# Kernel tuning notes

Hardware: AMD Instinct MI355X
Metric: run time of the kernel (lower is better)

The kernel has to match this reference:

```python
import jax, jax.numpy as jnp
import numpy as np

# 4D convolution via lax.conv_general_dilated with 4 spatial dims.
# Layout: input (N, C, D, H, W, T), kernel (O, I, d, h, w, t).
DN = ('NCDHWT', 'OIDHWT', 'NCDHWT')


def conv4d(x, w, b, pad):
    # torch Conv2d/Conv4d is cross-correlation, matching lax.conv_general_dilated
    y = jax.lax.conv_general_dilated(
        x, w, window_strides=(1, 1, 1, 1),
        padding=[(pad, pad)] * 4, dimension_numbers=DN)
    return y + b.reshape(1, -1, 1, 1, 1, 1)


def _kaiming(key, shape):
    fan_out = shape[0] * int(np.prod(shape[2:]))
    std = np.sqrt(2.0 / fan_out)
    return (jax.random.normal(key, shape, dtype=jnp.float32) * std).astype(jnp.float32)


def setup_inputs() -> dict:
    key = jax.random.key(0)
    ks = jax.random.split(key, 11)
    B, W, H = 256, 16, 16
    corr = jax.random.normal(ks[0], (B, W * H, W, H), dtype=jnp.float32)
    w1 = _kaiming(ks[1], (1, 1, 17, 17, 9, 9))
    w2 = _kaiming(ks[2], (1, 1, 7, 7, 7, 7))
    w3 = _kaiming(ks[3], (1, 1, 5, 5, 5, 5))
    w4 = _kaiming(ks[4], (1, 1, 3, 3, 3, 3))
    w5 = _kaiming(ks[5], (1, 1, 8, 8, 1, 1))
    b1 = jax.random.normal(ks[6], (1,), dtype=jnp.float32) * 0.01
    b2 = jax.random.normal(ks[7], (1,), dtype=jnp.float32) * 0.01
    b3 = jax.random.normal(ks[8], (1,), dtype=jnp.float32) * 0.01
    b4 = jax.random.normal(ks[9], (1,), dtype=jnp.float32) * 0.01
    b5 = jax.random.normal(ks[10], (1,), dtype=jnp.float32) * 0.01
    return {"corr": corr, "w1": w1, "b1": b1, "w2": w2, "b2": b2,
            "w3": w3, "b3": b3, "w4": w4, "b4": b4, "w5": w5, "b5": b5}


def reference(corr, w1, b1, w2, b2, w3, b3, w4, b4, w5, b5):
    B, HW, W, H = corr.shape
    x = corr.reshape(B, 1, W, H, W, H)          # (B,1,16,16,16,16)
    x = jax.nn.relu(conv4d(x, w1, b1, 4))       # (B,1, 8, 8,16,16)
    x = jax.nn.relu(conv4d(x, w2, b2, 3))
    x = jax.nn.relu(conv4d(x, w3, b3, 2))
    x = jax.nn.relu(conv4d(x, w4, b4, 1))
    out = jax.nn.sigmoid(conv4d(x, w5, b5, 0))  # (B,1, 1, 1,16,16)
    return out.reshape(B, 1, W, H)
```

## Files before the change

### kernel.cpp

```cpp
#include <hip/hip_runtime.h>
#include <math.h>


typedef short bf16x8 __attribute__((ext_vector_type(8)));
typedef float f32x4 __attribute__((ext_vector_type(4)));
typedef unsigned int u32x4 __attribute__((ext_vector_type(4)));

#define XTS 64
#define NROWS 396
#define ZROW 384
#define TTS 72

__device__ __forceinline__ int xts(int row, int col) {
  return row * XTS + (col ^ ((row & 7) << 3));
}

__device__ __forceinline__ unsigned short f2bf(float f) {
  unsigned int u = __float_as_uint(f);
  u += 0x7fffu + ((u >> 16) & 1u);
  return (unsigned short)(u >> 16);
}

template <int KSZ, int PAD>
__device__ __forceinline__ void build_mid(const float* __restrict__ w,
                                          unsigned short* __restrict__ Bg, int gid) {
  const int lane = gid & 63;
  const int n_tile = (gid >> 6) & 3;
  const int chunk = (gid >> 8) & 1;
  const int tap = gid >> 9;
  const int kw = tap / KSZ, kt = tap - kw * KSZ;
  const int dh_o = n_tile * 16 + (lane & 15);
  const int d_o = dh_o >> 3, h_o = dh_o & 7;
  const int kbase = chunk * 32 + (lane >> 4) * 8;
  unsigned int pk[4];
#pragma unroll
  for (int p = 0; p < 4; ++p) {
    unsigned short half[2];
#pragma unroll
    for (int s = 0; s < 2; ++s) {
      const int k = kbase + p * 2 + s;
      const int d_i = k >> 3, h_i = k & 7;
      const int kd = d_i - d_o + PAD, kh = h_i - h_o + PAD;
      float v = 0.f;
      if (kd >= 0 && kd < KSZ && kh >= 0 && kh < KSZ)
        v = w[((kd * KSZ + kh) * KSZ + kw) * KSZ + kt];
      half[s] = f2bf(v);
    }
    pk[p] = (unsigned int)half[0] | ((unsigned int)half[1] << 16);
  }
  *(int4*)(Bg + (size_t)gid * 8) = make_int4(pk[0], pk[1], pk[2], pk[3]);
}

__global__ __launch_bounds__(256) void build_all(const float* __restrict__ w1,
                                                 const float* __restrict__ w2,
                                                 const float* __restrict__ w3,
                                                 const float* __restrict__ w4,
                                                 unsigned short* __restrict__ Bg1,
                                                 unsigned short* __restrict__ Bg2,
                                                 unsigned short* __restrict__ Bg3,
                                                 unsigned short* __restrict__ Bg4) {
  const int bid = blockIdx.x, tid = threadIdx.x;
  if (bid < 648) {
    const int gid = bid * 256 + tid;
    const int lane = gid & 63;
    const int n_tile = (gid >> 6) & 3;
    const int chunk = (gid >> 8) & 7;
    const int kwkt = gid >> 11;
    const int kw = kwkt / 9, kt = kwkt - kw * 9;
    const int dh_o = n_tile * 16 + (lane & 15);
    const int d_o = dh_o >> 3, h_o = dh_o & 7;
    const int kbase = chunk * 32 + (lane >> 4) * 8;
    unsigned int pk[4];
#pragma unroll
    for (int p = 0; p < 4; ++p) {
      unsigned short half[2];
#pragma unroll
      for (int s = 0; s < 2; ++s) {
        const int k = kbase + p * 2 + s;
        const int d_i = k >> 4, h_i = k & 15;
        const int kd = d_i - d_o + 4, kh = h_i - h_o + 4;
        float v = 0.f;
        if (kd >= 0 && kd < 17 && kh >= 0 && kh < 17)
          v = w1[((kd * 17 + kh) * 9 + kw) * 9 + kt];
        half[s] = f2bf(v);
      }
      pk[p] = (unsigned int)half[0] | ((unsigned int)half[1] << 16);
    }
    *(int4*)(Bg1 + (size_t)gid * 8) = make_int4(pk[0], pk[1], pk[2], pk[3]);
  } else if (bid < 746) {
    build_mid<7, 3>(w2, Bg2, (bid - 648) * 256 + tid);
  } else if (bid < 796) {
    build_mid<5, 2>(w3, Bg3, (bid - 746) * 256 + tid);
  } else {
    build_mid<3, 1>(w4, Bg4, (bid - 796) * 256 + tid);
  }
}

__device__ __forceinline__ void l1_loadA(const unsigned short* XT, const int (&arb)[4],
                                         int kt, int tl, int quad, int chalf,
                                         bf16x8 (&A)[4]) {
  const int sw = ((tl + kt) & 7) << 3;
  const int c = (quad * 8 + chalf * 32) ^ sw;
  const int ko = kt * XTS;
#pragma unroll
  for (int m = 0; m < 4; ++m)
    A[m] = *(const bf16x8*)&XT[arb[m] + ko + c];
}

__device__ __forceinline__ void l1_loadB(const unsigned short* __restrict__ Bt, int kt,
                                         bf16x8 (&B)[8]) {
#pragma unroll
  for (int c = 0; c < 2; ++c)
#pragma unroll
    for (int n = 0; n < 4; ++n)
      B[c * 4 + n] = *(const bf16x8*)(Bt + (size_t)kt * 16384 + c * 2048 + n * 512);
}

__device__ __forceinline__ void mfma_half(const bf16x8 (&A)[4], const bf16x8* B,
                                          f32x4 (&acc)[4][4]) {
  __builtin_amdgcn_s_setprio(1);
#pragma unroll
  for (int m = 0; m < 4; ++m)
#pragma unroll
    for (int n = 0; n < 4; ++n)
      acc[m][n] = __builtin_amdgcn_mfma_f32_16x16x32_bf16(A[m], B[n], acc[m][n], 0, 0, 0);
  __builtin_amdgcn_s_setprio(0);
}

__global__ __launch_bounds__(256) void conv_l1_mfma(const float* __restrict__ x,
                                                    const unsigned short* __restrict__ Bg,
                                                    float* __restrict__ P) {
  __shared__ __align__(16) unsigned short XT[NROWS * XTS];
  const int bx = blockIdx.x;
  const int b = bx >> 1, khalf = bx & 1;
  const int tid = threadIdx.x;
  const int lane = tid & 63, wave = tid >> 6;
  const int quad = lane >> 4, tl = lane & 15;
  const float* xb = x + (size_t)b * 65536;
  f32x4 acc[4][4] = {};

  for (int j = tid; j < (NROWS * XTS) / 8; j += 256)
    *(int4*)&XT[j * 8] = make_int4(0, 0, 0, 0);
  __syncthreads();

  for (int qq = 0; qq < 2; ++qq) {
    const int q = khalf * 2 + qq;
    if (qq) __syncthreads();
#pragma unroll
    for (int it = 0; it < 8; ++it) {
      const int i = tid + it * 256;
      const int dhp = i >> 6, wtq = i & 63;
      const int r0 = (wtq >> 2) * 24 + (wtq & 3) * 4 + 4;
      const float4 ra = *(const float4*)(xb + (size_t)(q * 64 + 2 * dhp) * 256 + wtq * 4);
      const float4 rb =
          *(const float4*)(xb + (size_t)(q * 64 + 2 * dhp + 1) * 256 + wtq * 4);
      const float a0[4] = {ra.x, ra.y, ra.z, ra.w};
      const float a1[4] = {rb.x, rb.y, rb.z, rb.w};
#pragma unroll
      for (int j = 0; j < 4; ++j) {
        const unsigned int p = (unsigned int)f2bf(a0[j]) | ((unsigned int)f2bf(a1[j]) << 16);
        *(unsigned int*)&XT[xts(r0 + j, dhp * 2)] = p;
      }
    }
    __syncthreads();

    const unsigned short* Bt = Bg + (size_t)(q * 2) * 2048 + lane * 8;
    for (int kw = 0; kw < 9; ++kw) {
      int arb[4];
#pragma unroll
      for (int m = 0; m < 4; ++m) {
        const int w_i = wave * 4 + m + kw - 4;
        arb[m] = (((unsigned)w_i < 16u) ? (w_i * 24 + tl) : ZROW) * XTS;
      }
      bf16x8 B0[8], B1[8];
      l1_loadB(Bt, 0, B0);
#pragma unroll
      for (int kt = 0; kt < 9; ++kt) {
        bf16x8* Bc = (kt & 1) ? B1 : B0;
        bf16x8* Bn = (kt & 1) ? B0 : B1;
        if (kt < 8) l1_loadB(Bt, kt + 1, *(bf16x8(*)[8])Bn);
        bf16x8 A[4];
        l1_loadA(XT, arb, kt, tl, quad, 0, A);
        mfma_half(A, Bc, acc);
        l1_loadA(XT, arb, kt, tl, quad, 1, A);
        mfma_half(A, Bc + 4, acc);
      }
      Bt += 9 * 16384;
    }
  }

  float* Pb = P + (size_t)(khalf * 256 + b) * 16384;
#pragma unroll
  for (int m = 0; m < 4; ++m)
#pragma unroll
    for (int n = 0; n < 4; ++n) {
      const int dh_o = n * 16 + tl;
      const int wt0 = wave * 64 + m * 16 + quad * 4;
      *(float4*)&Pb[(size_t)dh_o * 256 + wt0] = *(const float4*)&acc[m][n];
    }
}

template <int KSZ, int PAD>
__device__ __forceinline__ void run_layer(unsigned short* XT,
                                          const unsigned short* __restrict__ Bg,
                                          const float bias, int mw, int nh, int lane,
                                          int quad, int tl) {
  f32x4 acc[4][2] = {};
  const unsigned short* BgL = Bg + lane * 8;
#pragma unroll
  for (int kt = 0; kt < KSZ; ++kt) {
    const int t_i = tl + kt - PAD;
    const bool tv = (unsigned)t_i < 16u;
    bf16x8 Aw[2][4];
#pragma unroll
    for (int m = 0; m < 4; ++m) {
      const int w_i = mw * 4 + m - PAD;
      const int row = (tv && (unsigned)w_i < 16u) ? (w_i * 16 + t_i) : 256;
      const int ro = row * TTS + quad * 8;
      Aw[0][m] = *(const bf16x8*)&XT[ro];
      Aw[1][m] = *(const bf16x8*)&XT[ro + 32];
    }
    bf16x8 Bb[2][4];
#pragma unroll
    for (int c = 0; c < 2; ++c)
#pragma unroll
      for (int n = 0; n < 2; ++n)
        Bb[0][c * 2 + n] =
            *(const bf16x8*)(BgL + (((size_t)(kt * 2 + c) * 4 + (nh * 2 + n)) << 9));
#pragma unroll
    for (int kw = 0; kw < KSZ; ++kw) {
      const int cur = kw & 1, nxt = cur ^ 1;
      if (kw + 1 < KSZ) {
        const int kwkt = (kw + 1) * KSZ + kt;
#pragma unroll
        for (int c = 0; c < 2; ++c)
#pragma unroll
          for (int n = 0; n < 2; ++n)
            Bb[nxt][c * 2 + n] =
                *(const bf16x8*)(BgL + (((size_t)(kwkt * 2 + c) * 4 + (nh * 2 + n)) << 9));
      }
      __builtin_amdgcn_s_setprio(1);
#pragma unroll
      for (int c = 0; c < 2; ++c)
#pragma unroll
        for (int m = 0; m < 4; ++m)
#pragma unroll
          for (int n = 0; n < 2; ++n)
            acc[m][n] = __builtin_amdgcn_mfma_f32_16x16x32_bf16(
                Aw[c][(kw + m) & 3], Bb[cur][c * 2 + n], acc[m][n], 0, 0, 0);
      __builtin_amdgcn_s_setprio(0);
      if (kw + 1 < KSZ) {
        const int w_i = mw * 4 + 4 + kw - PAD;
        const int row = (tv && (unsigned)w_i < 16u) ? (w_i * 16 + t_i) : 256;
        const int ro = row * TTS + quad * 8;
        Aw[0][kw & 3] = *(const bf16x8*)&XT[ro];
        Aw[1][kw & 3] = *(const bf16x8*)&XT[ro + 32];
      }
    }
  }
  __syncthreads();
#pragma unroll
  for (int m = 0; m < 4; ++m)
#pragma unroll
    for (int n = 0; n < 2; ++n) {
      const int col = (nh * 2 + n) * 16 + tl;
      const int wt0 = mw * 64 + m * 16 + quad * 4;
#pragma unroll
      for (int j = 0; j < 4; ++j)
        XT[(wt0 + j) * TTS + col] = f2bf(fmaxf(acc[m][n][j] + bias, 0.f));
    }
  __syncthreads();
}

__global__ __launch_bounds__(512) void tail_fused(const float* __restrict__ P,
                                                  const unsigned short* __restrict__ Bg2,
                                                  const unsigned short* __restrict__ Bg3,
                                                  const unsigned short* __restrict__ Bg4,
                                                  const float* __restrict__ b1,
                                                  const float* __restrict__ b2,
                                                  const float* __restrict__ b3,
                                                  const float* __restrict__ b4,
                                                  const float* __restrict__ w5,
                                                  const float* __restrict__ b5,
                                                  float* __restrict__ out) {
  __shared__ __align__(16) unsigned short XT[257 * TTS];
  const int b = blockIdx.x;
  const int tid = threadIdx.x;
  const int lane = tid & 63, wave = tid >> 6;
  const int quad = lane >> 4, tl = lane & 15;
  const int mw = wave >> 1, nh = wave & 1;
  const float* p0 = P + (size_t)b * 16384;
  const float* p1 = p0 + (size_t)256 * 16384;
  const float bias1 = b1[0];

  if (tid < 9) *(int4*)&XT[256 * TTS + tid * 8] = make_int4(0, 0, 0, 0);
#pragma unroll
  for (int it = 0; it < 4; ++it) {
    const int i = tid + it * 512;
    const int dhp = i >> 6, wtq = i & 63;
    const size_t off0 = (size_t)(2 * dhp) * 256 + wtq * 4;
    const float4 r0a = *(const float4*)(p0 + off0);
    const float4 r0b = *(const float4*)(p1 + off0);
    const float4 r1a = *(const float4*)(p0 + off0 + 256);
    const float4 r1b = *(const float4*)(p1 + off0 + 256);
    float a0[4] = {r0a.x + r0b.x, r0a.y + r0b.y, r0a.z + r0b.z, r0a.w + r0b.w};
    float a1[4] = {r1a.x + r1b.x, r1a.y + r1b.y, r1a.z + r1b.z, r1a.w + r1b.w};
#pragma unroll
    for (int j = 0; j < 4; ++j) {
      const unsigned short lo = f2bf(fmaxf(a0[j] + bias1, 0.f));
      const unsigned short hi = f2bf(fmaxf(a1[j] + bias1, 0.f));
      const unsigned int p = (unsigned int)lo | ((unsigned int)hi << 16);
      *(unsigned int*)&XT[(wtq * 4 + j) * TTS + dhp * 2] = p;
    }
  }
  __syncthreads();

  run_layer<7, 3>(XT, Bg2, b2[0], mw, nh, lane, quad, tl);
  run_layer<5, 2>(XT, Bg3, b3[0], mw, nh, lane, quad, tl);
  run_layer<3, 1>(XT, Bg4, b4[0], mw, nh, lane, quad, tl);

  if (tid < 256) {
    const int wt = tid;
    float s = b5[0];
    const unsigned short* row = &XT[wt * TTS];
#pragma unroll
    for (int k8 = 0; k8 < 8; ++k8) {
      const u32x4 v = *(const u32x4*)&row[k8 * 8];
      const unsigned int uu[4] = {(unsigned int)v.x, (unsigned int)v.y, (unsigned int)v.z,
                                  (unsigned int)v.w};
#pragma unroll
      for (int p = 0; p < 4; ++p) {
        const float lo = __uint_as_float(uu[p] << 16);
        const float hi = __uint_as_float(uu[p] & 0xFFFF0000u);
        s += lo * w5[k8 * 8 + p * 2] + hi * w5[k8 * 8 + p * 2 + 1];
      }
    }
    out[(size_t)b * 256 + wt] = 1.f / (1.f + expf(-s));
  }
}

extern "C" void kernel_launch(void* const* d_in, const int* in_sizes, int n_in,
                              void* d_out, int out_size, void* d_ws, size_t ws_size,
                              hipStream_t stream) {
  const float* corr = (const float*)d_in[0];
  const float* w1 = (const float*)d_in[1];
  const float* b1 = (const float*)d_in[2];
  const float* w2 = (const float*)d_in[3];
  const float* b2 = (const float*)d_in[4];
  const float* w3 = (const float*)d_in[5];
  const float* b3 = (const float*)d_in[6];
  const float* w4 = (const float*)d_in[7];
  const float* b4 = (const float*)d_in[8];
  const float* w5 = (const float*)d_in[9];
  const float* b5 = (const float*)d_in[10];

  float* P = (float*)d_ws;
  unsigned short* Bg1 = (unsigned short*)((char*)d_ws + (64u << 20));
  unsigned short* Bg2 = Bg1 + (size_t)81 * 8 * 4 * 64 * 8;
  unsigned short* Bg3 = Bg2 + (size_t)49 * 2 * 4 * 64 * 8;
  unsigned short* Bg4 = Bg3 + (size_t)25 * 2 * 4 * 64 * 8;

  build_all<<<814, 256, 0, stream>>>(w1, w2, w3, w4, Bg1, Bg2, Bg3, Bg4);
  conv_l1_mfma<<<512, 256, 0, stream>>>(corr, Bg1, P);
  tail_fused<<<256, 512, 0, stream>>>(P, Bg2, Bg3, Bg4, b1, b2, b3, b4, w5, b5,
                                      (float*)d_out);
}
```

Before: 257.7 us.

## Fuse layer-1 conv into tail kernel, dropping the split-K partial buffer

Merges the layer-1 MFMA conv into the fused tail kernel, one 512-thread block per batch element. The 8 waves split the output columns (nh) instead of splitting K across two blocks, and the layer-1 result goes straight to LDS as bf16. This removes the fp32 partial-sum write and read-back through global memory and one kernel launch. In exchange the grid drops from 512 to 256 blocks, each block runs all four K quarters serially, and the larger LDS footprint may reduce occupancy.

```diff
diff --git a/kernel.cpp b/kernel.cpp
--- a/kernel.cpp
+++ b/kernel.cpp
@@ -107,97 +107,24 @@
     A[m] = *(const bf16x8*)&XT[arb[m] + ko + c];
 }
 
-__device__ __forceinline__ void l1_loadB(const unsigned short* __restrict__ Bt, int kt,
-                                         bf16x8 (&B)[8]) {
+__device__ __forceinline__ void l1_loadB2(const unsigned short* __restrict__ Bt, int kt,
+                                          bf16x8 (&B)[4]) {
 #pragma unroll
   for (int c = 0; c < 2; ++c)
 #pragma unroll
-    for (int n = 0; n < 4; ++n)
-      B[c * 4 + n] = *(const bf16x8*)(Bt + (size_t)kt * 16384 + c * 2048 + n * 512);
-}
-
-__device__ __forceinline__ void mfma_half(const bf16x8 (&A)[4], const bf16x8* B,
-                                          f32x4 (&acc)[4][4]) {
+    for (int n = 0; n < 2; ++n)
+      B[c * 2 + n] = *(const bf16x8*)(Bt + (size_t)kt * 16384 + c * 2048 + n * 512);
+}
+
+__device__ __forceinline__ void mfma_half2(const bf16x8 (&A)[4], const bf16x8* B,
+                                           f32x4 (&acc)[4][2]) {
   __builtin_amdgcn_s_setprio(1);
 #pragma unroll
   for (int m = 0; m < 4; ++m)
 #pragma unroll
-    for (int n = 0; n < 4; ++n)
+    for (int n = 0; n < 2; ++n)
       acc[m][n] = __builtin_amdgcn_mfma_f32_16x16x32_bf16(A[m], B[n], acc[m][n], 0, 0, 0);
   __builtin_amdgcn_s_setprio(0);
-}
-
-__global__ __launch_bounds__(256) void conv_l1_mfma(const float* __restrict__ x,
-                                                    const unsigned short* __restrict__ Bg,
-                                                    float* __restrict__ P) {
-  __shared__ __align__(16) unsigned short XT[NROWS * XTS];
-  const int bx = blockIdx.x;
-  const int b = bx >> 1, khalf = bx & 1;
-  const int tid = threadIdx.x;
-  const int lane = tid & 63, wave = tid >> 6;
-  const int quad = lane >> 4, tl = lane & 15;
-  const float* xb = x + (size_t)b * 65536;
-  f32x4 acc[4][4] = {};
-
-  for (int j = tid; j < (NROWS * XTS) / 8; j += 256)
-    *(int4*)&XT[j * 8] = make_int4(0, 0, 0, 0);
-  __syncthreads();
-
-  for (int qq = 0; qq < 2; ++qq) {
-    const int q = khalf * 2 + qq;
-    if (qq) __syncthreads();
-#pragma unroll
-    for (int it = 0; it < 8; ++it) {
-      const int i = tid + it * 256;
-      const int dhp = i >> 6, wtq = i & 63;
-      const int r0 = (wtq >> 2) * 24 + (wtq & 3) * 4 + 4;
-      const float4 ra = *(const float4*)(xb + (size_t)(q * 64 + 2 * dhp) * 256 + wtq * 4);
-      const float4 rb =
-          *(const float4*)(xb + (size_t)(q * 64 + 2 * dhp + 1) * 256 + wtq * 4);
-      const float a0[4] = {ra.x, ra.y, ra.z, ra.w};
-      const float a1[4] = {rb.x, rb.y, rb.z, rb.w};
-#pragma unroll
-      for (int j = 0; j < 4; ++j) {
-        const unsigned int p = (unsigned int)f2bf(a0[j]) | ((unsigned int)f2bf(a1[j]) << 16);
-        *(unsigned int*)&XT[xts(r0 + j, dhp * 2)] = p;
-      }
-    }
-    __syncthreads();
-
-    const unsigned short* Bt = Bg + (size_t)(q * 2) * 2048 + lane * 8;
-    for (int kw = 0; kw < 9; ++kw) {
-      int arb[4];
-#pragma unroll
-      for (int m = 0; m < 4; ++m) {
-        const int w_i = wave * 4 + m + kw - 4;
-        arb[m] = (((unsigned)w_i < 16u) ? (w_i * 24 + tl) : ZROW) * XTS;
-      }
-      bf16x8 B0[8], B1[8];
-      l1_loadB(Bt, 0, B0);
-#pragma unroll
-      for (int kt = 0; kt < 9; ++kt) {
-        bf16x8* Bc = (kt & 1) ? B1 : B0;
-        bf16x8* Bn = (kt & 1) ? B0 : B1;
-        if (kt < 8) l1_loadB(Bt, kt + 1, *(bf16x8(*)[8])Bn);
-        bf16x8 A[4];
-        l1_loadA(XT, arb, kt, tl, quad, 0, A);
-        mfma_half(A, Bc, acc);
-        l1_loadA(XT, arb, kt, tl, quad, 1, A);
-        mfma_half(A, Bc + 4, acc);
-      }
-      Bt += 9 * 16384;
-    }
-  }
-
-  float* Pb = P + (size_t)(khalf * 256 + b) * 16384;
-#pragma unroll
-  for (int m = 0; m < 4; ++m)
-#pragma unroll
-    for (int n = 0; n < 4; ++n) {
-      const int dh_o = n * 16 + tl;
-      const int wt0 = wave * 64 + m * 16 + quad * 4;
-      *(float4*)&Pb[(size_t)dh_o * 256 + wt0] = *(const float4*)&acc[m][n];
-    }
 }
 
 template <int KSZ, int PAD>
@@ -272,52 +199,94 @@
   __syncthreads();
 }
 
-__global__ __launch_bounds__(512) void tail_fused(const float* __restrict__ P,
-                                                  const unsigned short* __restrict__ Bg2,
-                                                  const unsigned short* __restrict__ Bg3,
-                                                  const unsigned short* __restrict__ Bg4,
-                                                  const float* __restrict__ b1,
-                                                  const float* __restrict__ b2,
-                                                  const float* __restrict__ b3,
-                                                  const float* __restrict__ b4,
-                                                  const float* __restrict__ w5,
-                                                  const float* __restrict__ b5,
-                                                  float* __restrict__ out) {
-  __shared__ __align__(16) unsigned short XT[257 * TTS];
+__global__ __launch_bounds__(512) void net_fused(const float* __restrict__ x,
+                                                 const unsigned short* __restrict__ Bg1,
+                                                 const unsigned short* __restrict__ Bg2,
+                                                 const unsigned short* __restrict__ Bg3,
+                                                 const unsigned short* __restrict__ Bg4,
+                                                 const float* __restrict__ b1,
+                                                 const float* __restrict__ b2,
+                                                 const float* __restrict__ b3,
+                                                 const float* __restrict__ b4,
+                                                 const float* __restrict__ w5,
+                                                 const float* __restrict__ b5,
+                                                 float* __restrict__ out) {
+  __shared__ __align__(16) unsigned short XT[NROWS * XTS];
   const int b = blockIdx.x;
   const int tid = threadIdx.x;
   const int lane = tid & 63, wave = tid >> 6;
   const int quad = lane >> 4, tl = lane & 15;
-  const int mw = wave >> 1, nh = wave & 1;
-  const float* p0 = P + (size_t)b * 16384;
-  const float* p1 = p0 + (size_t)256 * 16384;
+  const int g = wave >> 1, nh = wave & 1;
+  const float* xb = x + (size_t)b * 65536;
   const float bias1 = b1[0];
-
+  f32x4 acc[4][2] = {};
+
+  for (int j = tid; j < (NROWS * XTS) / 8; j += 512)
+    *(int4*)&XT[j * 8] = make_int4(0, 0, 0, 0);
+  __syncthreads();
+
+  for (int q = 0; q < 4; ++q) {
+    if (q) __syncthreads();
+#pragma unroll
+    for (int it = 0; it < 4; ++it) {
+      const int i = tid + it * 512;
+      const int dhp = i >> 6, wtq = i & 63;
+      const int r0 = (wtq >> 2) * 24 + (wtq & 3) * 4 + 4;
+      const float4 ra = *(const float4*)(xb + (size_t)(q * 64 + 2 * dhp) * 256 + wtq * 4);
+      const float4 rb =
+          *(const float4*)(xb + (size_t)(q * 64 + 2 * dhp + 1) * 256 + wtq * 4);
+      const float a0[4] = {ra.x, ra.y, ra.z, ra.w};
+      const float a1[4] = {rb.x, rb.y, rb.z, rb.w};
+#pragma unroll
+      for (int j = 0; j < 4; ++j) {
+        const unsigned int p = (unsigned int)f2bf(a0[j]) | ((unsigned int)f2bf(a1[j]) << 16);
+        *(unsigned int*)&XT[xts(r0 + j, dhp * 2)] = p;
+      }
+    }
+    __syncthreads();
+
+    const unsigned short* Bt = Bg1 + (size_t)(q * 2) * 2048 + (nh * 2) * 512 + lane * 8;
+    for (int kw = 0; kw < 9; ++kw) {
+      int arb[4];
+#pragma unroll
+      for (int m = 0; m < 4; ++m) {
+        const int w_i = g * 4 + m + kw - 4;
+        arb[m] = (((unsigned)w_i < 16u) ? (w_i * 24 + tl) : ZROW) * XTS;
+      }
+      bf16x8 B0[4], B1[4];
+      l1_loadB2(Bt, 0, B0);
+#pragma unroll
+      for (int kt = 0; kt < 9; ++kt) {
+        bf16x8* Bc = (kt & 1) ? B1 : B0;
+        bf16x8* Bn = (kt & 1) ? B0 : B1;
+        if (kt < 8) l1_loadB2(Bt, kt + 1, *(bf16x8(*)[4])Bn);
+        bf16x8 A[4];
+        l1_loadA(XT, arb, kt, tl, quad, 0, A);
+        mfma_half2(A, Bc, acc);
+        l1_loadA(XT, arb, kt, tl, quad, 1, A);
+        mfma_half2(A, Bc + 2, acc);
+      }
+      Bt += 9 * 16384;
+    }
+  }
+  __syncthreads();
+
+#pragma unroll
+  for (int m = 0; m < 4; ++m)
+#pragma unroll
+    for (int n = 0; n < 2; ++n) {
+      const int col = (nh * 2 + n) * 16 + tl;
+      const int wt0 = g * 64 + m * 16 + quad * 4;
+#pragma unroll
+      for (int j = 0; j < 4; ++j)
+        XT[(wt0 + j) * TTS + col] = f2bf(fmaxf(acc[m][n][j] + bias1, 0.f));
+    }
   if (tid < 9) *(int4*)&XT[256 * TTS + tid * 8] = make_int4(0, 0, 0, 0);
-#pragma unroll
-  for (int it = 0; it < 4; ++it) {
-    const int i = tid + it * 512;
-    const int dhp = i >> 6, wtq = i & 63;
-    const size_t off0 = (size_t)(2 * dhp) * 256 + wtq * 4;
-    const float4 r0a = *(const float4*)(p0 + off0);
-    const float4 r0b = *(const float4*)(p1 + off0);
-    const float4 r1a = *(const float4*)(p0 + off0 + 256);
-    const float4 r1b = *(const float4*)(p1 + off0 + 256);
-    float a0[4] = {r0a.x + r0b.x, r0a.y + r0b.y, r0a.z + r0b.z, r0a.w + r0b.w};
-    float a1[4] = {r1a.x + r1b.x, r1a.y + r1b.y, r1a.z + r1b.z, r1a.w + r1b.w};
-#pragma unroll
-    for (int j = 0; j < 4; ++j) {
-      const unsigned short lo = f2bf(fmaxf(a0[j] + bias1, 0.f));
-      const unsigned short hi = f2bf(fmaxf(a1[j] + bias1, 0.f));
-      const unsigned int p = (unsigned int)lo | ((unsigned int)hi << 16);
-      *(unsigned int*)&XT[(wtq * 4 + j) * TTS + dhp * 2] = p;
-    }
-  }
-  __syncthreads();
-
-  run_layer<7, 3>(XT, Bg2, b2[0], mw, nh, lane, quad, tl);
-  run_layer<5, 2>(XT, Bg3, b3[0], mw, nh, lane, quad, tl);
-  run_layer<3, 1>(XT, Bg4, b4[0], mw, nh, lane, quad, tl);
+  __syncthreads();
+
+  run_layer<7, 3>(XT, Bg2, b2[0], g, nh, lane, quad, tl);
+  run_layer<5, 2>(XT, Bg3, b3[0], g, nh, lane, quad, tl);
+  run_layer<3, 1>(XT, Bg4, b4[0], g, nh, lane, quad, tl);
 
   if (tid < 256) {
     const int wt = tid;
@@ -354,14 +323,12 @@
   const float* w5 = (const float*)d_in[9];
   const float* b5 = (const float*)d_in[10];
 
-  float* P = (float*)d_ws;
-  unsigned short* Bg1 = (unsigned short*)((char*)d_ws + (64u << 20));
+  unsigned short* Bg1 = (unsigned short*)d_ws;
   unsigned short* Bg2 = Bg1 + (size_t)81 * 8 * 4 * 64 * 8;
   unsigned short* Bg3 = Bg2 + (size_t)49 * 2 * 4 * 64 * 8;
   unsigned short* Bg4 = Bg3 + (size_t)25 * 2 * 4 * 64 * 8;
 
   build_all<<<814, 256, 0, stream>>>(w1, w2, w3, w4, Bg1, Bg2, Bg3, Bg4);
-  conv_l1_mfma<<<512, 256, 0, stream>>>(corr, Bg1, P);
-  tail_fused<<<256, 512, 0, stream>>>(P, Bg2, Bg3, Bg4, b1, b2, b3, b4, w5, b5,
-                                      (float*)d_out);
-}
+  net_fused<<<256, 512, 0, stream>>>(corr, Bg1, Bg2, Bg3, Bg4, b1, b2, b3, b4, w5, b5,
+                                     (float*)d_out);
+}
```

Result: slower. 265.6 us (+3.0%).
